# Kernel optimization log

Measured on AMD Instinct MI355X. Metric: run time of the kernel, lower is better.

Reference implementation:

```python
import jax, jax.numpy as jnp
import numpy as np

N = 100000
E = 1600000
DIM_H = 128
NUM_HEADS = 8
HEAD_DIM = DIM_H // NUM_HEADS


def setup_inputs() -> dict:
    key = jax.random.key(0)
    ks = jax.random.split(key, 8)
    s = 1.0 / np.sqrt(DIM_H)
    return {
        "q": jax.random.normal(ks[0], (N, DIM_H), dtype=jnp.float32),
        "kv": jax.random.normal(ks[1], (N, DIM_H), dtype=jnp.float32),
        "edge_index": jax.random.randint(ks[2], (2, E), 0, N, dtype=jnp.int32),
        "W_k": jax.random.normal(ks[3], (DIM_H, DIM_H), dtype=jnp.float32) * s,
        "b_k": jnp.zeros((DIM_H,), dtype=jnp.float32),
        "W_v": jax.random.normal(ks[4], (DIM_H, DIM_H), dtype=jnp.float32) * s,
        "b_v": jnp.zeros((DIM_H,), dtype=jnp.float32),
        "W_o": jax.random.normal(ks[5], (DIM_H, DIM_H), dtype=jnp.float32) * s,
        "b_o": jnp.zeros((DIM_H,), dtype=jnp.float32),
    }


def reference(q, kv, edge_index, W_k, b_k, W_v, b_v, W_o, b_o):
    src, dst = edge_index[0], edge_index[1]
    # Projections: torch Linear is x @ W.T + b
    K = (kv @ W_k.T + b_k).reshape(N, NUM_HEADS, HEAD_DIM)
    V = (kv @ W_v.T + b_v).reshape(N, NUM_HEADS, HEAD_DIM)
    Q = q.reshape(N, NUM_HEADS, HEAD_DIM)

    # Edge-wise attention scores: [E, H]
    scores = jnp.sum(K[src] * Q[dst], axis=-1) / np.sqrt(HEAD_DIM)

    # Sparse softmax over incoming edges of each destination node
    seg_max = jax.ops.segment_max(scores, dst, num_segments=N)  # [N, H]
    ex = jnp.exp(scores - seg_max[dst])
    seg_sum = jax.ops.segment_sum(ex, dst, num_segments=N)  # [N, H]
    attn = ex / (seg_sum[dst] + 1e-16)  # [E, H]

    # Weighted message aggregation (dropout p=0.0 in eval -> identity)
    messages = V[src] * attn[:, :, None]  # [E, H, Hd]
    out = jax.ops.segment_sum(messages, dst, num_segments=N)  # [N, H, Hd]
    out = out.reshape(N, DIM_H)
    return out @ W_o.T + b_o
```

## Files before the change

kernel.cpp:

```cpp
#include <hip/hip_runtime.h>
#include <hip/hip_bf16.h>

#define N_NODES 100000
#define N_EDGES 1600000
#define DIM 128
#define NHEAD 8
#define HDIM 16

#define BSHIFT 9
#define BSZ 512
#define NB 196
#define S1_EDGES 4096

typedef __attribute__((ext_vector_type(8))) short short8;
typedef __attribute__((ext_vector_type(4))) float f32x4;

__device__ __forceinline__ unsigned short f2bf(float f) {
  union { __hip_bfloat16 h; unsigned short u; } c;
  c.h = __float2bfloat16(f);
  return c.u;
}

__global__ __launch_bounds__(256) void cvt3_kernel(const float* __restrict__ a,
                                                   const float* __restrict__ b,
                                                   const float* __restrict__ c,
                                                   unsigned short* __restrict__ y) {
  int i = blockIdx.x * 256 + threadIdx.x;
  const float* src = (i < 4096) ? a : ((i < 8192) ? b : c);
  int j = (i < 4096) ? i : ((i < 8192) ? i - 4096 : i - 8192);
  float4 v = ((const float4*)src)[j];
  ushort4 o;
  o.x = f2bf(v.x); o.y = f2bf(v.y); o.z = f2bf(v.z); o.w = f2bf(v.w);
  ((ushort4*)y)[i] = o;
}


__global__ __launch_bounds__(512) void bhist_kernel(const int* __restrict__ dst,
                                                    int* __restrict__ bcnt) {
  __shared__ int cnt[NB];
  int t = threadIdx.x;
  int base = blockIdx.x * S1_EDGES;
  if (t < NB) cnt[t] = 0;
  __syncthreads();
#pragma unroll
  for (int j = 0; j < S1_EDGES / 512; j++) {
    int e = base + j * 512 + t;
    if (e < N_EDGES) atomicAdd(&cnt[dst[e] >> BSHIFT], 1);
  }
  __syncthreads();
  if (t < NB) {
    int c = cnt[t];
    if (c) atomicAdd(&bcnt[t], c);
  }
}

__global__ __launch_bounds__(256) void bscan_kernel(const int* __restrict__ bcnt,
                                                    int* __restrict__ binBase,
                                                    int* __restrict__ binNext) {
  __shared__ int s[256];
  int t = threadIdx.x;
  int v = (t < NB) ? bcnt[t] : 0;
  s[t] = v;
  __syncthreads();
  for (int off = 1; off < 256; off <<= 1) {
    int x = (t >= off) ? s[t - off] : 0;
    __syncthreads();
    s[t] += x;
    __syncthreads();
  }
  int excl = (t == 0) ? 0 : s[t - 1];
  if (t <= NB) binBase[t] = excl;
  if (t < NB) binNext[t] = excl;
}

__global__ __launch_bounds__(512) void bin_kernel(const int* __restrict__ src,
                                                  const int* __restrict__ dst,
                                                  int* __restrict__ binNext,
                                                  unsigned* __restrict__ binned) {
  __shared__ unsigned pk[S1_EDGES];
  __shared__ unsigned char bkt[S1_EDGES];
  __shared__ int cnt[NB], gb[NB], ln[NB];
  int t = threadIdx.x;
  int base = blockIdx.x * S1_EDGES;
  if (t < NB) { cnt[t] = 0; ln[t] = 0; }
  __syncthreads();
#pragma unroll
  for (int j = 0; j < S1_EDGES / 512; j++) {
    int idx = j * 512 + t;
    int e = base + idx;
    if (e < N_EDGES) {
      int s = src[e], d = dst[e];
      int bb = d >> BSHIFT;
      pk[idx] = (unsigned)s | ((unsigned)(d & (BSZ - 1)) << 17);
      bkt[idx] = (unsigned char)bb;
      atomicAdd(&cnt[bb], 1);
    } else {
      bkt[idx] = 0xFF;
    }
  }
  __syncthreads();
  if (t < NB) {
    int c = cnt[t];
    gb[t] = c ? atomicAdd(&binNext[t], c) : 0;
  }
  __syncthreads();
#pragma unroll
  for (int j = 0; j < S1_EDGES / 512; j++) {
    int idx = j * 512 + t;
    int bb = bkt[idx];
    if (bb != 0xFF) {
      int r = atomicAdd(&ln[bb], 1);
      binned[gb[bb] + r] = pk[idx];
    }
  }
}

__global__ __launch_bounds__(512) void fine_kernel(const unsigned* __restrict__ binned,
                                                   const int* __restrict__ binBase,
                                                   int* __restrict__ rowptr,
                                                   int* __restrict__ esrc) {
  __shared__ int cnt[BSZ], sc[BSZ], nxt[BSZ];
  int b = blockIdx.x, t = threadIdx.x;
  int beg = binBase[b], end = binBase[b + 1];
  cnt[t] = 0;
  __syncthreads();
  for (int i = beg + t; i < end; i += 512) atomicAdd(&cnt[binned[i] >> 17], 1);
  __syncthreads();
  int v = cnt[t];
  sc[t] = v;
  __syncthreads();
  for (int off = 1; off < 512; off <<= 1) {
    int x = (t >= off) ? sc[t - off] : 0;
    __syncthreads();
    sc[t] += x;
    __syncthreads();
  }
  int pos = beg + sc[t] - v;
  int node = b * BSZ + t;
  if (node <= N_NODES) rowptr[node] = pos;
  nxt[t] = pos;
  __syncthreads();
  for (int i = beg + t; i < end; i += 512) {
    unsigned p = binned[i];
    int r = atomicAdd(&nxt[p >> 17], 1);
    esrc[r] = (int)(p & 0x1FFFFu);
  }
}

__global__ __launch_bounds__(256) void kv_proj_mfma(const float* __restrict__ A,
                                                    const unsigned short* __restrict__ Wk,
                                                    const float* __restrict__ bk,
                                                    const unsigned short* __restrict__ Wv,
                                                    const float* __restrict__ bv,
                                                    unsigned short* __restrict__ KV, int n) {
  __shared__ unsigned short tile[64][264];
  int w = threadIdx.x >> 6, lane = threadIdx.x & 63;
  int m = lane & 15, quad = lane >> 4;
  int rbase = blockIdx.x * 64 + w * 16;
  int arow = rbase + m;
  if (arow >= n) arow = n - 1;
  const float* ap = A + (size_t)arow * DIM + quad * 8;
  short8 af[4];
#pragma unroll
  for (int t = 0; t < 4; t++) {
    float4 lo = *(const float4*)(ap + 32 * t);
    float4 hi = *(const float4*)(ap + 32 * t + 4);
    short8 f;
    f[0] = (short)f2bf(lo.x); f[1] = (short)f2bf(lo.y);
    f[2] = (short)f2bf(lo.z); f[3] = (short)f2bf(lo.w);
    f[4] = (short)f2bf(hi.x); f[5] = (short)f2bf(hi.y);
    f[6] = (short)f2bf(hi.z); f[7] = (short)f2bf(hi.w);
    af[t] = f;
  }
#pragma unroll
  for (int ct = 0; ct < 16; ct++) {
    const unsigned short* W = (ct < 8) ? Wk : Wv;
    const float* bias = (ct < 8) ? bk : bv;
    int c0 = (ct & 7) * 16;
    const unsigned short* wp = W + (size_t)(c0 + m) * DIM + quad * 8;
    f32x4 acc = {0.f, 0.f, 0.f, 0.f};
    acc = __builtin_amdgcn_mfma_f32_16x16x32_bf16(af[0], *(const short8*)(wp), acc, 0, 0, 0);
    acc = __builtin_amdgcn_mfma_f32_16x16x32_bf16(af[1], *(const short8*)(wp + 32), acc, 0, 0, 0);
    acc = __builtin_amdgcn_mfma_f32_16x16x32_bf16(af[2], *(const short8*)(wp + 64), acc, 0, 0, 0);
    acc = __builtin_amdgcn_mfma_f32_16x16x32_bf16(af[3], *(const short8*)(wp + 96), acc, 0, 0, 0);
    float bb = bias[c0 + m];
    int c = c0 + m;
    int pos = ((ct < 8) ? 0 : 4) + (c >> 2) * 8 + (c & 3);
    int lr = w * 16 + quad * 4;
#pragma unroll
    for (int r = 0; r < 4; r++) tile[lr + r][pos] = f2bf(acc[r] + bb);
  }
  __syncthreads();
#pragma unroll
  for (int it = 0; it < 8; it++) {
    int cidx = it * 256 + threadIdx.x;
    int row = cidx >> 5;
    int off = (cidx & 31) * 8;
    int g = blockIdx.x * 64 + row;
    if (g < n)
      *(uint4*)(KV + (size_t)g * 256 + off) = *(const uint4*)(&tile[row][off]);
  }
}

__global__ __launch_bounds__(256) void o_proj_mfma(const unsigned short* __restrict__ A,
                                                   const unsigned short* __restrict__ Wo,
                                                   const float* __restrict__ bo,
                                                   float* __restrict__ out, int n) {
  int w = threadIdx.x >> 6, lane = threadIdx.x & 63;
  int m = lane & 15, quad = lane >> 4;
  int rbase = blockIdx.x * 64 + w * 16;
  int arow = rbase + m;
  if (arow >= n) arow = n - 1;
  const unsigned short* ap = A + (size_t)arow * DIM + quad * 8;
  short8 af0 = *(const short8*)(ap);
  short8 af1 = *(const short8*)(ap + 32);
  short8 af2 = *(const short8*)(ap + 64);
  short8 af3 = *(const short8*)(ap + 96);
#pragma unroll
  for (int ct = 0; ct < 8; ct++) {
    int c0 = ct * 16;
    const unsigned short* wp = Wo + (size_t)(c0 + m) * DIM + quad * 8;
    f32x4 acc = {0.f, 0.f, 0.f, 0.f};
    acc = __builtin_amdgcn_mfma_f32_16x16x32_bf16(af0, *(const short8*)(wp), acc, 0, 0, 0);
    acc = __builtin_amdgcn_mfma_f32_16x16x32_bf16(af1, *(const short8*)(wp + 32), acc, 0, 0, 0);
    acc = __builtin_amdgcn_mfma_f32_16x16x32_bf16(af2, *(const short8*)(wp + 64), acc, 0, 0, 0);
    acc = __builtin_amdgcn_mfma_f32_16x16x32_bf16(af3, *(const short8*)(wp + 96), acc, 0, 0, 0);
    float bb = bo[c0 + m];
#pragma unroll
    for (int r = 0; r < 4; r++) {
      int rr = rbase + quad * 4 + r;
      if (rr < n) out[(size_t)rr * DIM + c0 + m] = acc[r] + bb;
    }
  }
}

__global__ __launch_bounds__(256) void attn_kernel(const float* __restrict__ q,
                                                   const unsigned short* __restrict__ KV,
                                                   const int* __restrict__ rowptr,
                                                   const int* __restrict__ esrc,
                                                   unsigned short* __restrict__ pre) {
  int wid = blockIdx.x * 4 + __builtin_amdgcn_readfirstlane(threadIdx.x >> 6);
  int lane = threadIdx.x & 63;
  int half = lane >> 5;
  int p = lane & 31;
  const float SCALE = 0.25f * 1.44269504088896340736f;
  float4 qv = *(const float4*)(q + (size_t)wid * DIM + p * 4);
  float qx = qv.x * SCALE, qy = qv.y * SCALE, qz = qv.z * SCALE, qw = qv.w * SCALE;
  const unsigned short* base = KV + p * 8;

  float l = 0.f, o0 = 0.f, o1 = 0.f, o2 = 0.f, o3 = 0.f;
  int beg = rowptr[wid], end = rowptr[wid + 1];

#define EDGE2(d, wgt)                                                        \
  {                                                                          \
    float k0 = __uint_as_float((d).x << 16);                                 \
    float k1 = __uint_as_float((d).x & 0xffff0000u);                         \
    float k2 = __uint_as_float((d).y << 16);                                 \
    float k3 = __uint_as_float((d).y & 0xffff0000u);                         \
    float part = fmaf(k1, qy, k0 * qx);                                      \
    part = fmaf(k3, qw, fmaf(k2, qz, part));                                 \
    part += __shfl_xor(part, 1);                                             \
    part += __shfl_xor(part, 2);                                             \
    float e = exp2f(part) * (wgt);                                           \
    l += e;                                                                  \
    o0 = fmaf(e, __uint_as_float((d).z << 16), o0);                          \
    o1 = fmaf(e, __uint_as_float((d).z & 0xffff0000u), o1);                  \
    o2 = fmaf(e, __uint_as_float((d).w << 16), o2);                          \
    o3 = fmaf(e, __uint_as_float((d).w & 0xffff0000u), o3);                  \
  }

  int i = beg;
  for (; i + 8 <= end; i += 8) {
    int4 sa = *(const int4*)(esrc + i);
    int4 sb = *(const int4*)(esrc + i + 4);
    int s0 = half ? sa.y : sa.x;
    int s1 = half ? sa.w : sa.z;
    int s2 = half ? sb.y : sb.x;
    int s3 = half ? sb.w : sb.z;
    uint4 d0 = *(const uint4*)(base + (size_t)s0 * 256);
    uint4 d1 = *(const uint4*)(base + (size_t)s1 * 256);
    uint4 d2 = *(const uint4*)(base + (size_t)s2 * 256);
    uint4 d3 = *(const uint4*)(base + (size_t)s3 * 256);
    EDGE2(d0, 1.f) EDGE2(d1, 1.f) EDGE2(d2, 1.f) EDGE2(d3, 1.f)
  }
  for (; i + 2 <= end; i += 2) {
    int s = esrc[i + half];
    uint4 d = *(const uint4*)(base + (size_t)s * 256);
    EDGE2(d, 1.f)
  }
  if (i < end) {
    int s = esrc[i];
    uint4 d = *(const uint4*)(base + (size_t)s * 256);
    float hm = half ? 0.f : 1.f;
    EDGE2(d, hm)
  }
#undef EDGE2

  l += __shfl_xor(l, 32);
  o0 += __shfl_xor(o0, 32);
  o1 += __shfl_xor(o1, 32);
  o2 += __shfl_xor(o2, 32);
  o3 += __shfl_xor(o3, 32);

  float inv = __builtin_amdgcn_rcpf(l + 1e-16f);
  if (half == 0) {
    ushort4 r;
    r.x = f2bf(o0 * inv);
    r.y = f2bf(o1 * inv);
    r.z = f2bf(o2 * inv);
    r.w = f2bf(o3 * inv);
    *(ushort4*)(pre + (size_t)wid * DIM + p * 4) = r;
  }
}


extern "C" void kernel_launch(void* const* d_in, const int* in_sizes, int n_in,
                              void* d_out, int out_size, void* d_ws, size_t ws_size,
                              hipStream_t stream) {
  const float* q  = (const float*)d_in[0];
  const float* kv = (const float*)d_in[1];
  const int* ei   = (const int*)d_in[2];
  const float* Wk = (const float*)d_in[3];
  const float* bk = (const float*)d_in[4];
  const float* Wv = (const float*)d_in[5];
  const float* bv = (const float*)d_in[6];
  const float* Wo = (const float*)d_in[7];
  const float* bo = (const float*)d_in[8];
  float* out = (float*)d_out;
  const int* srcp = ei;
  const int* dstp = ei + N_EDGES;

  char* ws = (char*)d_ws;
  size_t o = 0;
  auto alloc = [&](size_t bytes) {
    void* p = ws + o;
    o += (bytes + 511) & ~(size_t)511;
    return p;
  };
  unsigned short* Wkb = (unsigned short*)alloc((size_t)DIM * DIM * 2);
  unsigned short* Wvb = (unsigned short*)alloc((size_t)DIM * DIM * 2);
  unsigned short* Wob = (unsigned short*)alloc((size_t)DIM * DIM * 2);
  unsigned short* KV  = (unsigned short*)alloc((size_t)N_NODES * 256 * 2);
  unsigned short* pre = (unsigned short*)alloc((size_t)N_NODES * DIM * 2);
  int* esrc      = (int*)alloc((size_t)N_EDGES * 4);
  unsigned* binned = (unsigned*)alloc((size_t)N_EDGES * 4);
  int* rowptr    = (int*)alloc((size_t)(N_NODES + 1) * 4);
  int* bcnt      = (int*)alloc((size_t)NB * 4);
  int* binBase   = (int*)alloc((size_t)(NB + 1) * 4);
  int* binNext   = (int*)alloc((size_t)NB * 4);
  (void)ws_size;

  hipMemsetAsync(bcnt, 0, (size_t)NB * 4, stream);
  cvt3_kernel<<<48, 256, 0, stream>>>(Wk, Wv, Wo, Wkb);
  int nbblk = (N_EDGES + S1_EDGES - 1) / S1_EDGES;
  bhist_kernel<<<nbblk, 512, 0, stream>>>(dstp, bcnt);
  bscan_kernel<<<1, 256, 0, stream>>>(bcnt, binBase, binNext);
  bin_kernel<<<nbblk, 512, 0, stream>>>(srcp, dstp, binNext, binned);
  fine_kernel<<<NB, 512, 0, stream>>>(binned, binBase, rowptr, esrc);
  kv_proj_mfma<<<(N_NODES + 63) / 64, 256, 0, stream>>>(kv, Wkb, bk, Wvb, bv, KV, N_NODES);
  attn_kernel<<<N_NODES / 4, 256, 0, stream>>>(q, KV, rowptr, esrc, pre);
  o_proj_mfma<<<(N_NODES + 63) / 64, 256, 0, stream>>>(pre, Wob, bo, out, N_NODES);
}
```

Baseline: 386.6 us.

## Fuse attention aggregation with output projection via shared-memory tile

Merges the attention kernel and the output-projection GEMM into one kernel: each block processes 16 destination nodes, with waves pulling nodes dynamically through an LDS atomic counter, stores the normalized bf16 results in a shared tile, then runs MFMA against Wo. This removes the global round-trip of the intermediate 'pre' buffer and one kernel launch. In exchange each block now waits at a barrier for its slowest node before the GEMM. The work is split across two launches of 3125 blocks each.

```diff
diff --git a/kernel.cpp b/kernel.cpp
--- a/kernel.cpp
+++ b/kernel.cpp
@@ -202,54 +202,36 @@
   }
 }
 
-__global__ __launch_bounds__(256) void o_proj_mfma(const unsigned short* __restrict__ A,
-                                                   const unsigned short* __restrict__ Wo,
-                                                   const float* __restrict__ bo,
-                                                   float* __restrict__ out, int n) {
-  int w = threadIdx.x >> 6, lane = threadIdx.x & 63;
-  int m = lane & 15, quad = lane >> 4;
-  int rbase = blockIdx.x * 64 + w * 16;
-  int arow = rbase + m;
-  if (arow >= n) arow = n - 1;
-  const unsigned short* ap = A + (size_t)arow * DIM + quad * 8;
-  short8 af0 = *(const short8*)(ap);
-  short8 af1 = *(const short8*)(ap + 32);
-  short8 af2 = *(const short8*)(ap + 64);
-  short8 af3 = *(const short8*)(ap + 96);
-#pragma unroll
-  for (int ct = 0; ct < 8; ct++) {
-    int c0 = ct * 16;
-    const unsigned short* wp = Wo + (size_t)(c0 + m) * DIM + quad * 8;
-    f32x4 acc = {0.f, 0.f, 0.f, 0.f};
-    acc = __builtin_amdgcn_mfma_f32_16x16x32_bf16(af0, *(const short8*)(wp), acc, 0, 0, 0);
-    acc = __builtin_amdgcn_mfma_f32_16x16x32_bf16(af1, *(const short8*)(wp + 32), acc, 0, 0, 0);
-    acc = __builtin_amdgcn_mfma_f32_16x16x32_bf16(af2, *(const short8*)(wp + 64), acc, 0, 0, 0);
-    acc = __builtin_amdgcn_mfma_f32_16x16x32_bf16(af3, *(const short8*)(wp + 96), acc, 0, 0, 0);
-    float bb = bo[c0 + m];
-#pragma unroll
-    for (int r = 0; r < 4; r++) {
-      int rr = rbase + quad * 4 + r;
-      if (rr < n) out[(size_t)rr * DIM + c0 + m] = acc[r] + bb;
-    }
-  }
-}
-
-__global__ __launch_bounds__(256) void attn_kernel(const float* __restrict__ q,
-                                                   const unsigned short* __restrict__ KV,
-                                                   const int* __restrict__ rowptr,
-                                                   const int* __restrict__ esrc,
-                                                   unsigned short* __restrict__ pre) {
-  int wid = blockIdx.x * 4 + __builtin_amdgcn_readfirstlane(threadIdx.x >> 6);
-  int lane = threadIdx.x & 63;
-  int half = lane >> 5;
-  int p = lane & 31;
+__global__ __launch_bounds__(256) void attn_oproj_kernel(const float* __restrict__ q,
+                                                         const unsigned short* __restrict__ KV,
+                                                         const int* __restrict__ rowptr,
+                                                         const int* __restrict__ esrc,
+                                                         const unsigned short* __restrict__ Wo,
+                                                         const float* __restrict__ bo,
+                                                         float* __restrict__ out,
+                                                         int nodeBase) {
+  __shared__ unsigned short tile[16][136];
+  __shared__ int nextT;
+  int tid = threadIdx.x;
+  int wlane = tid & 63;
+  int half = wlane >> 5;
+  int p = wlane & 31;
+  if (tid == 0) nextT = 0;
+  __syncthreads();
+  int rowBase = nodeBase + blockIdx.x * 16;
   const float SCALE = 0.25f * 1.44269504088896340736f;
-  float4 qv = *(const float4*)(q + (size_t)wid * DIM + p * 4);
-  float qx = qv.x * SCALE, qy = qv.y * SCALE, qz = qv.z * SCALE, qw = qv.w * SCALE;
   const unsigned short* base = KV + p * 8;
 
-  float l = 0.f, o0 = 0.f, o1 = 0.f, o2 = 0.f, o3 = 0.f;
-  int beg = rowptr[wid], end = rowptr[wid + 1];
+  for (;;) {
+    int t;
+    if (wlane == 0) t = atomicAdd(&nextT, 1);
+    t = __shfl(t, 0);
+    if (t >= 16) break;
+    int wid = rowBase + t;
+    float4 qv = *(const float4*)(q + (size_t)wid * DIM + p * 4);
+    float qx = qv.x * SCALE, qy = qv.y * SCALE, qz = qv.z * SCALE, qw = qv.w * SCALE;
+    float l = 0.f, o0 = 0.f, o1 = 0.f, o2 = 0.f, o3 = 0.f;
+    int beg = rowptr[wid], end = rowptr[wid + 1];
 
 #define EDGE2(d, wgt)                                                        \
   {                                                                          \
@@ -269,47 +251,73 @@
     o3 = fmaf(e, __uint_as_float((d).w & 0xffff0000u), o3);                  \
   }
 
-  int i = beg;
-  for (; i + 8 <= end; i += 8) {
-    int4 sa = *(const int4*)(esrc + i);
-    int4 sb = *(const int4*)(esrc + i + 4);
-    int s0 = half ? sa.y : sa.x;
-    int s1 = half ? sa.w : sa.z;
-    int s2 = half ? sb.y : sb.x;
-    int s3 = half ? sb.w : sb.z;
-    uint4 d0 = *(const uint4*)(base + (size_t)s0 * 256);
-    uint4 d1 = *(const uint4*)(base + (size_t)s1 * 256);
-    uint4 d2 = *(const uint4*)(base + (size_t)s2 * 256);
-    uint4 d3 = *(const uint4*)(base + (size_t)s3 * 256);
-    EDGE2(d0, 1.f) EDGE2(d1, 1.f) EDGE2(d2, 1.f) EDGE2(d3, 1.f)
-  }
-  for (; i + 2 <= end; i += 2) {
-    int s = esrc[i + half];
-    uint4 d = *(const uint4*)(base + (size_t)s * 256);
-    EDGE2(d, 1.f)
-  }
-  if (i < end) {
-    int s = esrc[i];
-    uint4 d = *(const uint4*)(base + (size_t)s * 256);
-    float hm = half ? 0.f : 1.f;
-    EDGE2(d, hm)
-  }
+    int i = beg;
+    for (; i + 8 <= end; i += 8) {
+      int4 sa = *(const int4*)(esrc + i);
+      int4 sb = *(const int4*)(esrc + i + 4);
+      int s0 = half ? sa.y : sa.x;
+      int s1 = half ? sa.w : sa.z;
+      int s2 = half ? sb.y : sb.x;
+      int s3 = half ? sb.w : sb.z;
+      uint4 d0 = *(const uint4*)(base + (size_t)s0 * 256);
+      uint4 d1 = *(const uint4*)(base + (size_t)s1 * 256);
+      uint4 d2 = *(const uint4*)(base + (size_t)s2 * 256);
+      uint4 d3 = *(const uint4*)(base + (size_t)s3 * 256);
+      EDGE2(d0, 1.f) EDGE2(d1, 1.f) EDGE2(d2, 1.f) EDGE2(d3, 1.f)
+    }
+    for (; i + 2 <= end; i += 2) {
+      int s = esrc[i + half];
+      uint4 d = *(const uint4*)(base + (size_t)s * 256);
+      EDGE2(d, 1.f)
+    }
+    if (i < end) {
+      int s = esrc[i];
+      uint4 d = *(const uint4*)(base + (size_t)s * 256);
+      float hm = half ? 0.f : 1.f;
+      EDGE2(d, hm)
+    }
 #undef EDGE2
 
-  l += __shfl_xor(l, 32);
-  o0 += __shfl_xor(o0, 32);
-  o1 += __shfl_xor(o1, 32);
-  o2 += __shfl_xor(o2, 32);
-  o3 += __shfl_xor(o3, 32);
-
-  float inv = __builtin_amdgcn_rcpf(l + 1e-16f);
-  if (half == 0) {
-    ushort4 r;
-    r.x = f2bf(o0 * inv);
-    r.y = f2bf(o1 * inv);
-    r.z = f2bf(o2 * inv);
-    r.w = f2bf(o3 * inv);
-    *(ushort4*)(pre + (size_t)wid * DIM + p * 4) = r;
+    l += __shfl_xor(l, 32);
+    o0 += __shfl_xor(o0, 32);
+    o1 += __shfl_xor(o1, 32);
+    o2 += __shfl_xor(o2, 32);
+    o3 += __shfl_xor(o3, 32);
+
+    float inv = __builtin_amdgcn_rcpf(l + 1e-16f);
+    if (half == 0) {
+      ushort4 r4;
+      r4.x = f2bf(o0 * inv);
+      r4.y = f2bf(o1 * inv);
+      r4.z = f2bf(o2 * inv);
+      r4.w = f2bf(o3 * inv);
+      *(ushort4*)(&tile[t][p * 4]) = r4;
+    }
+  }
+  __syncthreads();
+
+  int w = tid >> 6;
+  int m = wlane & 15, quad = wlane >> 4;
+  short8 af0 = *(const short8*)(&tile[m][quad * 8]);
+  short8 af1 = *(const short8*)(&tile[m][quad * 8 + 32]);
+  short8 af2 = *(const short8*)(&tile[m][quad * 8 + 64]);
+  short8 af3 = *(const short8*)(&tile[m][quad * 8 + 96]);
+#pragma unroll
+  for (int c2 = 0; c2 < 2; c2++) {
+    int ct = w * 2 + c2;
+    int c0 = ct * 16;
+    const unsigned short* wp = Wo + (size_t)(c0 + m) * DIM + quad * 8;
+    f32x4 acc = {0.f, 0.f, 0.f, 0.f};
+    acc = __builtin_amdgcn_mfma_f32_16x16x32_bf16(af0, *(const short8*)(wp), acc, 0, 0, 0);
+    acc = __builtin_amdgcn_mfma_f32_16x16x32_bf16(af1, *(const short8*)(wp + 32), acc, 0, 0, 0);
+    acc = __builtin_amdgcn_mfma_f32_16x16x32_bf16(af2, *(const short8*)(wp + 64), acc, 0, 0, 0);
+    acc = __builtin_amdgcn_mfma_f32_16x16x32_bf16(af3, *(const short8*)(wp + 96), acc, 0, 0, 0);
+    float bb = bo[c0 + m];
+#pragma unroll
+    for (int r = 0; r < 4; r++) {
+      int rr = rowBase + quad * 4 + r;
+      out[(size_t)rr * DIM + c0 + m] = acc[r] + bb;
+    }
   }
 }
 
@@ -341,7 +349,6 @@
   unsigned short* Wvb = (unsigned short*)alloc((size_t)DIM * DIM * 2);
   unsigned short* Wob = (unsigned short*)alloc((size_t)DIM * DIM * 2);
   unsigned short* KV  = (unsigned short*)alloc((size_t)N_NODES * 256 * 2);
-  unsigned short* pre = (unsigned short*)alloc((size_t)N_NODES * DIM * 2);
   int* esrc      = (int*)alloc((size_t)N_EDGES * 4);
   unsigned* binned = (unsigned*)alloc((size_t)N_EDGES * 4);
   int* rowptr    = (int*)alloc((size_t)(N_NODES + 1) * 4);
@@ -358,6 +365,6 @@
   bin_kernel<<<nbblk, 512, 0, stream>>>(srcp, dstp, binNext, binned);
   fine_kernel<<<NB, 512, 0, stream>>>(binned, binBase, rowptr, esrc);
   kv_proj_mfma<<<(N_NODES + 63) / 64, 256, 0, stream>>>(kv, Wkb, bk, Wvb, bv, KV, N_NODES);
-  attn_kernel<<<N_NODES / 4, 256, 0, stream>>>(q, KV, rowptr, esrc, pre);
-  o_proj_mfma<<<(N_NODES + 63) / 64, 256, 0, stream>>>(pre, Wob, bo, out, N_NODES);
-}
+  attn_oproj_kernel<<<3125, 256, 0, stream>>>(q, KV, rowptr, esrc, Wob, bo, out, 0);
+  attn_oproj_kernel<<<3125, 256, 0, stream>>>(q, KV, rowptr, esrc, Wob, bo, out, 50000);
+}
```

New measurement: 385.3 us. About the same (-0.3%).

## Halve bucket size, record ranks in first pass, cache bins in LDS

Applied to the files above, without the earlier changes.

The coarse bucket size for the two-pass counting sort of edges by destination drops from 512 to 256 nodes, giving 391 bins, so the fine kernel launches about twice as many blocks. The bin kernel now records each edge's rank from the first atomic pass and reuses it, which removes the second round of shared-memory atomics. The fine kernel keeps its bin's edges in a 32KB LDS cache instead of reading global memory twice. The larger LDS footprint may lower occupancy, and bins with more than 8192 edges fall back to global reads.

```diff
diff --git a/kernel.cpp b/kernel.cpp
--- a/kernel.cpp
+++ b/kernel.cpp
@@ -7,9 +7,9 @@
 #define NHEAD 8
 #define HDIM 16
 
-#define BSHIFT 9
-#define BSZ 512
-#define NB 196
+#define BSHIFT 8
+#define BSZ 256
+#define NB 391
 #define S1_EDGES 4096
 
 typedef __attribute__((ext_vector_type(8))) short short8;
@@ -40,7 +40,7 @@
   __shared__ int cnt[NB];
   int t = threadIdx.x;
   int base = blockIdx.x * S1_EDGES;
-  if (t < NB) cnt[t] = 0;
+  for (int j = t; j < NB; j += 512) cnt[j] = 0;
   __syncthreads();
 #pragma unroll
   for (int j = 0; j < S1_EDGES / 512; j++) {
@@ -48,21 +48,21 @@
     if (e < N_EDGES) atomicAdd(&cnt[dst[e] >> BSHIFT], 1);
   }
   __syncthreads();
-  if (t < NB) {
-    int c = cnt[t];
-    if (c) atomicAdd(&bcnt[t], c);
-  }
-}
-
-__global__ __launch_bounds__(256) void bscan_kernel(const int* __restrict__ bcnt,
+  for (int j = t; j < NB; j += 512) {
+    int c = cnt[j];
+    if (c) atomicAdd(&bcnt[j], c);
+  }
+}
+
+__global__ __launch_bounds__(512) void bscan_kernel(const int* __restrict__ bcnt,
                                                     int* __restrict__ binBase,
                                                     int* __restrict__ binNext) {
-  __shared__ int s[256];
+  __shared__ int s[512];
   int t = threadIdx.x;
   int v = (t < NB) ? bcnt[t] : 0;
   s[t] = v;
   __syncthreads();
-  for (int off = 1; off < 256; off <<= 1) {
+  for (int off = 1; off < 512; off <<= 1) {
     int x = (t >= off) ? s[t - off] : 0;
     __syncthreads();
     s[t] += x;
@@ -78,11 +78,12 @@
                                                   int* __restrict__ binNext,
                                                   unsigned* __restrict__ binned) {
   __shared__ unsigned pk[S1_EDGES];
-  __shared__ unsigned char bkt[S1_EDGES];
-  __shared__ int cnt[NB], gb[NB], ln[NB];
+  __shared__ unsigned short bbv[S1_EDGES];
+  __shared__ unsigned short rk[S1_EDGES];
+  __shared__ int cnt[NB], gb[NB];
   int t = threadIdx.x;
   int base = blockIdx.x * S1_EDGES;
-  if (t < NB) { cnt[t] = 0; ln[t] = 0; }
+  for (int j = t; j < NB; j += 512) cnt[j] = 0;
   __syncthreads();
 #pragma unroll
   for (int j = 0; j < S1_EDGES / 512; j++) {
@@ -92,26 +93,23 @@
       int s = src[e], d = dst[e];
       int bb = d >> BSHIFT;
       pk[idx] = (unsigned)s | ((unsigned)(d & (BSZ - 1)) << 17);
-      bkt[idx] = (unsigned char)bb;
-      atomicAdd(&cnt[bb], 1);
+      bbv[idx] = (unsigned short)bb;
+      rk[idx] = (unsigned short)atomicAdd(&cnt[bb], 1);
     } else {
-      bkt[idx] = 0xFF;
+      bbv[idx] = 0xFFFF;
     }
   }
   __syncthreads();
-  if (t < NB) {
-    int c = cnt[t];
-    gb[t] = c ? atomicAdd(&binNext[t], c) : 0;
+  for (int j = t; j < NB; j += 512) {
+    int c = cnt[j];
+    gb[j] = c ? atomicAdd(&binNext[j], c) : 0;
   }
   __syncthreads();
 #pragma unroll
   for (int j = 0; j < S1_EDGES / 512; j++) {
     int idx = j * 512 + t;
-    int bb = bkt[idx];
-    if (bb != 0xFF) {
-      int r = atomicAdd(&ln[bb], 1);
-      binned[gb[bb] + r] = pk[idx];
-    }
+    unsigned short bb = bbv[idx];
+    if (bb != 0xFFFF) binned[gb[bb] + rk[idx]] = pk[idx];
   }
 }
 
@@ -119,29 +117,37 @@
                                                    const int* __restrict__ binBase,
                                                    int* __restrict__ rowptr,
                                                    int* __restrict__ esrc) {
+  __shared__ unsigned cache[8192];
   __shared__ int cnt[BSZ], sc[BSZ], nxt[BSZ];
   int b = blockIdx.x, t = threadIdx.x;
   int beg = binBase[b], end = binBase[b + 1];
-  cnt[t] = 0;
-  __syncthreads();
-  for (int i = beg + t; i < end; i += 512) atomicAdd(&cnt[binned[i] >> 17], 1);
-  __syncthreads();
-  int v = cnt[t];
-  sc[t] = v;
-  __syncthreads();
-  for (int off = 1; off < 512; off <<= 1) {
-    int x = (t >= off) ? sc[t - off] : 0;
-    __syncthreads();
-    sc[t] += x;
-    __syncthreads();
-  }
-  int pos = beg + sc[t] - v;
-  int node = b * BSZ + t;
-  if (node <= N_NODES) rowptr[node] = pos;
-  nxt[t] = pos;
+  bool useCache = (end - beg) <= 8192;
+  if (t < BSZ) cnt[t] = 0;
   __syncthreads();
   for (int i = beg + t; i < end; i += 512) {
     unsigned p = binned[i];
+    if (useCache) cache[i - beg] = p;
+    atomicAdd(&cnt[p >> 17], 1);
+  }
+  __syncthreads();
+  int v = (t < BSZ) ? cnt[t] : 0;
+  if (t < BSZ) sc[t] = v;
+  __syncthreads();
+  for (int off = 1; off < BSZ; off <<= 1) {
+    int x = (t >= off && t < BSZ) ? sc[t - off] : 0;
+    __syncthreads();
+    if (t < BSZ) sc[t] += x;
+    __syncthreads();
+  }
+  if (t < BSZ) {
+    int pos = beg + sc[t] - v;
+    int node = b * BSZ + t;
+    if (node <= N_NODES) rowptr[node] = pos;
+    nxt[t] = pos;
+  }
+  __syncthreads();
+  for (int i = beg + t; i < end; i += 512) {
+    unsigned p = useCache ? cache[i - beg] : binned[i];
     int r = atomicAdd(&nxt[p >> 17], 1);
     esrc[r] = (int)(p & 0x1FFFFu);
   }
@@ -354,7 +360,7 @@
   cvt3_kernel<<<48, 256, 0, stream>>>(Wk, Wv, Wo, Wkb);
   int nbblk = (N_EDGES + S1_EDGES - 1) / S1_EDGES;
   bhist_kernel<<<nbblk, 512, 0, stream>>>(dstp, bcnt);
-  bscan_kernel<<<1, 256, 0, stream>>>(bcnt, binBase, binNext);
+  bscan_kernel<<<1, 512, 0, stream>>>(bcnt, binBase, binNext);
   bin_kernel<<<nbblk, 512, 0, stream>>>(srcp, dstp, binNext, binned);
   fine_kernel<<<NB, 512, 0, stream>>>(binned, binBase, rowptr, esrc);
   kv_proj_mfma<<<(N_NODES + 63) / 64, 256, 0, stream>>>(kv, Wkb, bk, Wvb, bv, KV, N_NODES);
```

After: 388.7 us. About the same (+0.6%).
